# Kernel tuning notes

Measured on AMD Instinct MI355X. Metric: run time of the kernel, lower is better.

Reference implementation:

```python
import jax, jax.numpy as jnp
import numpy as np

ROUNDS = 64   # sequential hash rounds
HIDDEN = 256  # state width (bits) and square matrix size
B = 65536     # batch of independent inputs being hashed in parallel


def setup_inputs() -> dict:
    key = jax.random.key(0)
    k1, k2, k3 = jax.random.split(key, 3)
    # state bits in {0,1}, shape [B, HIDDEN]
    state = jax.random.randint(k1, (B, HIDDEN), 0, 2).astype(jnp.float32)
    # ternary matrices in {-1,0,1} (bytes % 3 - 1 in the original), [ROUNDS, HIDDEN, HIDDEN]
    matrices = (jax.random.randint(k2, (ROUNDS, HIDDEN, HIDDEN), 0, 3) - 1).astype(jnp.float32)
    # per-round noise bits in {0,1}, [ROUNDS, HIDDEN]
    noise = jax.random.randint(k3, (ROUNDS, HIDDEN), 0, 2).astype(jnp.float32)
    return {"state": state, "matrices": matrices, "noise": noise}


def reference(state, matrices, noise):
    # Each round: state = floor(state @ W_r^T + noise_r) mod 2
    def step(s, wn):
        W, n = wn  # W: [HIDDEN, HIDDEN], n: [HIDDEN]
        s = jnp.remainder(jnp.floor(jnp.matmul(s, W.T) + n), 2.0)
        return s, None

    out, _ = jax.lax.scan(step, state, (matrices, noise))
    return out  # [B, HIDDEN] final bit state
```

## Files before the change

kernel.cpp:

```cpp
#include <hip/hip_runtime.h>
#include <stdint.h>

#define ROUNDS 64
#define HIDDEN 256
#define BATCH  65536
#define NSUP   16

typedef int   v4i  __attribute__((ext_vector_type(4)));
typedef int   v8i  __attribute__((ext_vector_type(8)));
typedef float v16f __attribute__((ext_vector_type(16)));
typedef unsigned long long u64;


#define WB_OFF   0u
#define NB_OFF   524288u
#define WPK_OFF  526336u
#define NF_OFF   1050624u

__host__ __device__ constexpr int rho(int n) {
  return 4 * (n >> 4) + (n & 3) + 8 * ((n >> 2) & 3);
}

__host__ __device__ constexpr float bias_q(int q) {
  return (q == 0) ? 6291456.0f
       : (q == 1) ? 393216.0f
       : (q == 2) ? 24576.0f
                  : 1536.0f;
}

__global__ __launch_bounds__(256) void bitpack(const float* __restrict__ mat,
                                               const float* __restrict__ noi,
                                               u64* __restrict__ wb,
                                               u64* __restrict__ nb) {
  unsigned blk = blockIdx.x;
  if (blk >= 16384u) {
    unsigned tg = (blk - 16384u) * 256u + threadIdx.x;
    u64 m = __ballot(noi[tg] != 0.f);
    if ((threadIdx.x & 63u) == 0u) nb[tg >> 6] = m;
    return;
  }
  unsigned tg = blk * 256u + threadIdx.x;
  u64 m = __ballot(mat[tg] != 0.f);
  if ((threadIdx.x & 63u) == 0u) wb[tg >> 6] = m;
}

__device__ __forceinline__ void fold_stream(u64 (&A)[256][5],
                                            u64 (&tbl)[64][16][5],
                                            u64 (&avec)[4],
                                            const u64* __restrict__ inM,
                                            const u64* __restrict__ inV,
                                            int base, int count,
                                            int tid, int w, int i) {
  A[i][w] = inM[(size_t)base * 1024 + i * 4 + w];
  if (tid < 4) avec[tid] = inV[base * 4 + tid];
  u64 brP[4];
  u64 bwP;
  {
    const u64* Bm = inM + (size_t)(base + 1) * 1024;
#pragma unroll
    for (int q = 0; q < 4; ++q) brP[q] = Bm[i * 4 + q];
    bwP = (tid < 256) ? inV[(size_t)(base + 1) * 4 + (i >> 6)] : 0ull;
  }
  __syncthreads();

  for (int j = 1; j < count; ++j) {
    const u64 br0 = brP[0], br1 = brP[1], br2 = brP[2], br3 = brP[3];
    const u64 bwc = bwP;
    if (j + 1 < count) {
      const u64* Bm = inM + (size_t)(base + j + 1) * 1024;
#pragma unroll
      for (int q = 0; q < 4; ++q) brP[q] = Bm[i * 4 + q];
      bwP = (tid < 256) ? inV[(size_t)(base + j + 1) * 4 + (i >> 6)] : 0ull;
    }
    u64 av0 = avec[0], av1 = avec[1], av2 = avec[2], av3 = avec[3];

    {
      const int c = tid >> 4, m = tid & 15;
      u64 t0 = 0, t1 = 0, t2 = 0, t3 = 0;
#pragma unroll
      for (int jj = 0; jj < 4; ++jj)
        if (m & (1 << jj)) {
          t0 ^= A[4 * c + jj][0]; t1 ^= A[4 * c + jj][1];
          t2 ^= A[4 * c + jj][2]; t3 ^= A[4 * c + jj][3];
        }
      tbl[c][m][0] = t0; tbl[c][m][1] = t1; tbl[c][m][2] = t2; tbl[c][m][3] = t3;
    }
    __syncthreads();

    const u64 brr[4] = {br0, br1, br2, br3};
    u64 a0 = 0, a1 = 0, a2 = 0, a3 = 0;
#pragma unroll
    for (int c = 0; c < 64; c += 4) {
      unsigned n0 = (unsigned)(brr[(c + 0) >> 4] >> (((c + 0) & 15) * 4)) & 15u;
      unsigned n1 = (unsigned)(brr[(c + 1) >> 4] >> (((c + 1) & 15) * 4)) & 15u;
      unsigned n2 = (unsigned)(brr[(c + 2) >> 4] >> (((c + 2) & 15) * 4)) & 15u;
      unsigned n3 = (unsigned)(brr[(c + 3) >> 4] >> (((c + 3) & 15) * 4)) & 15u;
      a0 ^= tbl[c + 0][n0][w];
      a1 ^= tbl[c + 1][n1][w];
      a2 ^= tbl[c + 2][n2][w];
      a3 ^= tbl[c + 3][n3][w];
    }
    u64 acc = (a0 ^ a1) ^ (a2 ^ a3);

    u64 mask = 0;
    if (tid < 256) {
      int p = __popcll(br0 & av0) + __popcll(br1 & av1) +
              __popcll(br2 & av2) + __popcll(br3 & av3);
      int bit = ((int)((bwc >> (i & 63)) & 1ull)) ^ (p & 1);
      mask = __ballot(bit);
    }
    __syncthreads();
    A[i][w] = acc;
    if (tid < 256 && (i & 63) == 0) avec[i >> 6] = mask;
    __syncthreads();
  }
}

__global__ __launch_bounds__(1024) void fold16(const u64* __restrict__ wb,
                                               const u64* __restrict__ nb,
                                               uint32_t* __restrict__ wpk,
                                               float* __restrict__ nf) {
  __shared__ u64 A[256][5];
  __shared__ u64 tbl[64][16][5];
  __shared__ u64 avec[4];
  const int tid = threadIdx.x;
  const int g = blockIdx.x;

  fold_stream(A, tbl, avec, wb, nb, 4 * g, 4, tid, tid >> 8, tid & 255);

#pragma unroll
  for (int it = 0; it < 2; ++it) {
    unsigned tg = (unsigned)it * 1024u + tid;
    unsigned kwin = tg & 7u, row = tg >> 3;
    uint32_t wd[4] = {0, 0, 0, 0};
#pragma unroll
    for (int n = 0; n < 32; ++n) {
      int k = (int)kwin * 32 + rho(n);
      uint32_t bit = (uint32_t)((A[row][k >> 6] >> (k & 63)) & 1ull);
      wd[n >> 3] |= (bit * 2u) << ((n & 7) * 4);
    }
    unsigned mt = row >> 5, lhh = kwin & 1u, ks = kwin >> 1;
    unsigned lane = lhh * 32u + (row & 31u);
    *(uint4*)(wpk + ((((unsigned)g * 32u + mt * 4u + ks) * 64u + lane) << 2)) =
        make_uint4(wd[0], wd[1], wd[2], wd[3]);
  }
  if (tid < 256) {
    unsigned j = tid & 15u, lhh = (tid >> 4) & 1u, mt = (unsigned)tid >> 5;
    unsigned row = mt * 32u + (j & 3u) + 8u * (j >> 2) + 4u * lhh;
    nf[(unsigned)g * 256u + tid] = (float)((avec[row >> 6] >> (row & 63u)) & 1ull);
  }
}

__global__ __launch_bounds__(512, 4) void hash16(const uint32_t* __restrict__ wpk,
                                                 const float* __restrict__ nf,
                                                 const float* __restrict__ sta,
                                                 float* __restrict__ out) {
  __shared__ uint8_t T[2][8][128][16];
  const int t = threadIdx.x;
  const int wv = __builtin_amdgcn_readfirstlane(t >> 6);
  const int lane = t & 63;
  const int l31 = lane & 31;
  const int lh = lane >> 5;
  const int el0 = blockIdx.x * 128;

#pragma unroll
  for (int i = 0; i < 16; ++i) {
    unsigned flat = (unsigned)i * 512u + t;
    unsigned el = flat >> 6, k4 = flat & 63u;
    float4 f = ((const float4*)(sta + (size_t)el0 * 256))[flat];
    uint32_t v = ((f.x != 0.f) ? 0x2u : 0u) | ((f.y != 0.f) ? 0x20u : 0u) |
                 ((f.z != 0.f) ? 0x200u : 0u) | ((f.w != 0.f) ? 0x2000u : 0u);
    unsigned KB = k4 >> 3, k4c = k4 & 7u;
    unsigned byteoff = (k4c & 1u) * 8u + 2u * (k4c >> 1);
    *(uint16_t*)&T[0][KB][el][byteoff] = (uint16_t)v;
  }
  __syncthreads();

  v4i ap[4];
  {
    const uint32_t* wb = wpk + ((wv * 4) << 8);
#pragma unroll
    for (int ks = 0; ks < 4; ++ks) ap[ks] = *(const v4i*)(wb + ks * 256 + lane * 4);
  }
  v16f NZ = *(const v16f*)(nf + (wv * 2 + lh) * 16);

  for (int r = 0; r < NSUP; ++r) {
    const int rb = r & 1, nx = rb ^ 1;
    v16f acc[4];
    __builtin_amdgcn_s_setprio(1);
#pragma unroll
    for (int ks = 0; ks < 4; ++ks) {
      v8i A8 = __builtin_shufflevector(ap[ks], ap[ks], 0, 1, 2, 3, -1, -1, -1, -1);
      const int kb = 2 * ks + lh;
#pragma unroll
      for (int tn = 0; tn < 4; ++tn) {
        v4i b4 = *(const v4i*)&T[rb][kb][tn * 32 + l31][0];
        v8i B8 = __builtin_shufflevector(b4, b4, 0, 1, 2, 3, -1, -1, -1, -1);
        acc[tn] = __builtin_amdgcn_mfma_scale_f32_32x32x64_f8f6f4(
            A8, B8, (ks == 0) ? NZ : acc[tn], 4, 4, 0, 127, 0, 127);
      }
    }
    __builtin_amdgcn_s_setprio(0);

    {
      const int rn = (r + 1) & (NSUP - 1);
      const uint32_t* wb = wpk + (((rn * 8 + wv) * 4) << 8);
#pragma unroll
      for (int ks = 0; ks < 4; ++ks) ap[ks] = *(const v4i*)(wb + ks * 256 + lane * 4);
      NZ = *(const v16f*)(nf + ((rn * 8 + wv) * 2 + lh) * 16);
    }

#pragma unroll
    for (int tn = 0; tn < 4; ++tn) {
#define PB(j)                                                          \
  (__builtin_bit_cast(uint32_t, acc[tn][j] + bias_q((j) & 3)) &        \
   (2u << (4 * ((j) & 3))))
      uint32_t u0 = PB(0) | PB(1) | PB(2) | PB(3);
      uint32_t u1 = PB(4) | PB(5) | PB(6) | PB(7);
      uint32_t u2 = PB(8) | PB(9) | PB(10) | PB(11);
      uint32_t u3 = PB(12) | PB(13) | PB(14) | PB(15);
#undef PB
      *(uint2*)&T[nx][wv][tn * 32 + l31][lh * 8] =
          make_uint2(u0 | (u1 << 16), u2 | (u3 << 16));
    }

    __syncthreads();
  }

#pragma unroll
  for (int i = 0; i < 16; ++i) {
    unsigned flat = (unsigned)i * 512u + t;
    unsigned el = flat >> 6, k4 = flat & 63u;
    unsigned KB = k4 >> 3, k4c = k4 & 7u;
    unsigned byteoff = (k4c & 1u) * 8u + 2u * (k4c >> 1);
    uint32_t v = *(const uint16_t*)&T[0][KB][el][byteoff];
    float4 o = make_float4((float)((v >> 1) & 1u), (float)((v >> 5) & 1u),
                           (float)((v >> 9) & 1u), (float)((v >> 13) & 1u));
    ((float4*)(out + (size_t)el0 * 256))[flat] = o;
  }
}

extern "C" void kernel_launch(void* const* d_in, const int* in_sizes, int n_in,
                              void* d_out, int out_size, void* d_ws, size_t ws_size,
                              hipStream_t stream) {
  const float* sta = (const float*)d_in[0];
  const float* mat = (const float*)d_in[1];
  const float* noi = (const float*)d_in[2];
  uint8_t* wsb = (uint8_t*)d_ws;

  u64* Wb       = (u64*)(wsb + WB_OFF);
  u64* nb       = (u64*)(wsb + NB_OFF);
  uint32_t* wpk = (uint32_t*)(wsb + WPK_OFF);
  float* nf     = (float*)(wsb + NF_OFF);

  bitpack<<<16448, 256, 0, stream>>>(mat, noi, Wb, nb);
  fold16<<<16, 1024, 0, stream>>>(Wb, nb, wpk, nf);
  hash16<<<512, 512, 0, stream>>>(wpk, nf, sta, (float*)d_out);
}
```

Baseline: 207.2 us.

## Fuse matrix/noise bit-packing into the fold kernel and drop the intermediate buffer

Removes the separate bitpack kernel and has each of the 16 fold blocks ballot-pack its own four rounds of float matrices and noise directly into shared memory. This saves a kernel launch and the global write and read of the packed bit matrices. The fold loop now reads the next operand from shared memory instead of prefetching it from global memory. The trade-off is that the 16 MB float matrix read now runs on only 16 workgroups, where before it was spread across the whole GPU, so it may be bandwidth-limited per CU.

New measurement: 273.7 us. +32.1%, slower.

```diff
diff --git a/kernel.cpp b/kernel.cpp
--- a/kernel.cpp
+++ b/kernel.cpp
@@ -12,10 +12,8 @@
 typedef unsigned long long u64;
 
 
-#define WB_OFF   0u
-#define NB_OFF   524288u
-#define WPK_OFF  526336u
-#define NF_OFF   1050624u
+#define WPK_OFF  0u
+#define NF_OFF   524288u
 
 __host__ __device__ constexpr int rho(int n) {
   return 4 * (n >> 4) + (n & 3) + 8 * ((n >> 2) & 3);
@@ -28,51 +26,43 @@
                   : 1536.0f;
 }
 
-__global__ __launch_bounds__(256) void bitpack(const float* __restrict__ mat,
-                                               const float* __restrict__ noi,
-                                               u64* __restrict__ wb,
-                                               u64* __restrict__ nb) {
-  unsigned blk = blockIdx.x;
-  if (blk >= 16384u) {
-    unsigned tg = (blk - 16384u) * 256u + threadIdx.x;
-    u64 m = __ballot(noi[tg] != 0.f);
-    if ((threadIdx.x & 63u) == 0u) nb[tg >> 6] = m;
-    return;
-  }
-  unsigned tg = blk * 256u + threadIdx.x;
-  u64 m = __ballot(mat[tg] != 0.f);
-  if ((threadIdx.x & 63u) == 0u) wb[tg >> 6] = m;
-}
-
-__device__ __forceinline__ void fold_stream(u64 (&A)[256][5],
-                                            u64 (&tbl)[64][16][5],
-                                            u64 (&avec)[4],
-                                            const u64* __restrict__ inM,
-                                            const u64* __restrict__ inV,
-                                            int base, int count,
-                                            int tid, int w, int i) {
-  A[i][w] = inM[(size_t)base * 1024 + i * 4 + w];
-  if (tid < 4) avec[tid] = inV[base * 4 + tid];
-  u64 brP[4];
-  u64 bwP;
+__global__ __launch_bounds__(1024) void foldpack16(const float* __restrict__ mat,
+                                                   const float* __restrict__ noi,
+                                                   uint32_t* __restrict__ wpk,
+                                                   float* __restrict__ nf) {
+  __shared__ u64 WB[4][256][5];
+  __shared__ u64 NBv[4][4];
+  __shared__ u64 A[256][5];
+  __shared__ u64 tbl[64][16][5];
+  __shared__ u64 avec[4];
+  const int tid = threadIdx.x;
+  const int g = blockIdx.x;
+  const int w = tid >> 8;
+  const int i = tid & 255;
+
   {
-    const u64* Bm = inM + (size_t)(base + 1) * 1024;
-#pragma unroll
-    for (int q = 0; q < 4; ++q) brP[q] = Bm[i * 4 + q];
-    bwP = (tid < 256) ? inV[(size_t)(base + 1) * 4 + (i >> 6)] : 0ull;
+    const float* src = mat + (size_t)g * 262144;
+#pragma unroll 8
+    for (int it = 0; it < 256; ++it) {
+      unsigned e = (unsigned)it * 1024u + (unsigned)tid;
+      u64 m = __ballot(src[e] != 0.f);
+      if ((tid & 63) == 0) WB[e >> 16][(e >> 8) & 255][(e >> 6) & 3] = m;
+    }
+    u64 m = __ballot(noi[(size_t)g * 1024 + tid] != 0.f);
+    if ((tid & 63) == 0) NBv[tid >> 8][(tid >> 6) & 3] = m;
   }
   __syncthreads();
 
-  for (int j = 1; j < count; ++j) {
-    const u64 br0 = brP[0], br1 = brP[1], br2 = brP[2], br3 = brP[3];
-    const u64 bwc = bwP;
-    if (j + 1 < count) {
-      const u64* Bm = inM + (size_t)(base + j + 1) * 1024;
-#pragma unroll
-      for (int q = 0; q < 4; ++q) brP[q] = Bm[i * 4 + q];
-      bwP = (tid < 256) ? inV[(size_t)(base + j + 1) * 4 + (i >> 6)] : 0ull;
-    }
-    u64 av0 = avec[0], av1 = avec[1], av2 = avec[2], av3 = avec[3];
+  A[i][w] = WB[0][i][w];
+  if (tid < 4) avec[tid] = NBv[0][tid];
+  __syncthreads();
+
+#pragma unroll
+  for (int j = 1; j < 4; ++j) {
+    const u64 br0 = WB[j][i][0], br1 = WB[j][i][1],
+              br2 = WB[j][i][2], br3 = WB[j][i][3];
+    const u64 bwc = NBv[j][i >> 6];
+    const u64 av0 = avec[0], av1 = avec[1], av2 = avec[2], av3 = avec[3];
 
     {
       const int c = tid >> 4, m = tid & 15;
@@ -100,7 +90,7 @@
       a2 ^= tbl[c + 2][n2][w];
       a3 ^= tbl[c + 3][n3][w];
     }
-    u64 acc = (a0 ^ a1) ^ (a2 ^ a3);
+    const u64 acc = (a0 ^ a1) ^ (a2 ^ a3);
 
     u64 mask = 0;
     if (tid < 256) {
@@ -114,19 +104,6 @@
     if (tid < 256 && (i & 63) == 0) avec[i >> 6] = mask;
     __syncthreads();
   }
-}
-
-__global__ __launch_bounds__(1024) void fold16(const u64* __restrict__ wb,
-                                               const u64* __restrict__ nb,
-                                               uint32_t* __restrict__ wpk,
-                                               float* __restrict__ nf) {
-  __shared__ u64 A[256][5];
-  __shared__ u64 tbl[64][16][5];
-  __shared__ u64 avec[4];
-  const int tid = threadIdx.x;
-  const int g = blockIdx.x;
-
-  fold_stream(A, tbl, avec, wb, nb, 4 * g, 4, tid, tid >> 8, tid & 255);
 
 #pragma unroll
   for (int it = 0; it < 2; ++it) {
@@ -248,12 +225,9 @@
   const float* noi = (const float*)d_in[2];
   uint8_t* wsb = (uint8_t*)d_ws;
 
-  u64* Wb       = (u64*)(wsb + WB_OFF);
-  u64* nb       = (u64*)(wsb + NB_OFF);
   uint32_t* wpk = (uint32_t*)(wsb + WPK_OFF);
   float* nf     = (float*)(wsb + NF_OFF);
 
-  bitpack<<<16448, 256, 0, stream>>>(mat, noi, Wb, nb);
-  fold16<<<16, 1024, 0, stream>>>(Wb, nb, wpk, nf);
+  foldpack16<<<16, 1024, 0, stream>>>(mat, noi, wpk, nf);
   hash16<<<512, 512, 0, stream>>>(wpk, nf, sta, (float*)d_out);
 }
```

## Fold eight rounds per affine map and prepack state bits in bitpack kernel

Applied to the files above, without the earlier changes.

Each folded affine map now composes 8 rounds instead of 4, so the hash kernel runs 8 super-rounds of MFMA work instead of 16 and the fold kernel runs 8 blocks each folding 8 rounds. The state bit extraction moves into the bitpack launch, producing packed 32-bit words that the hash kernel spreads into its LDS layout with bit tricks instead of reading the float state itself. The trade-offs are a longer serial fold chain per block, an extra packed buffer in the workspace, and extra blocks in bitpack.

New measurement: 229.6 us. 1.11x slower.

```diff
diff --git a/kernel.cpp b/kernel.cpp
--- a/kernel.cpp
+++ b/kernel.cpp
@@ -4,7 +4,7 @@
 #define ROUNDS 64
 #define HIDDEN 256
 #define BATCH  65536
-#define NSUP   16
+#define NSUP   8
 
 typedef int   v4i  __attribute__((ext_vector_type(4)));
 typedef int   v8i  __attribute__((ext_vector_type(8)));
@@ -12,10 +12,11 @@
 typedef unsigned long long u64;
 
 
-#define WB_OFF   0u
-#define NB_OFF   524288u
-#define WPK_OFF  526336u
-#define NF_OFF   1050624u
+#define SPK_OFF  0u
+#define WB_OFF   2097152u
+#define NB_OFF   2621440u
+#define WPK_OFF  2623488u
+#define NF_OFF   2885632u
 
 __host__ __device__ constexpr int rho(int n) {
   return 4 * (n >> 4) + (n & 3) + 8 * ((n >> 2) & 3);
@@ -28,20 +29,49 @@
                   : 1536.0f;
 }
 
+__device__ __forceinline__ u64 spread16(uint32_t p) {
+  u64 t = p;
+  t = (t | (t << 24)) & 0x000000FF000000FFull;
+  t = (t | (t << 12)) & 0x000F000F000F000Full;
+  t = (t | (t << 6))  & 0x0303030303030303ull;
+  t = (t | (t << 3))  & 0x1111111111111111ull;
+  return t << 1;
+}
+
 __global__ __launch_bounds__(256) void bitpack(const float* __restrict__ mat,
                                                const float* __restrict__ noi,
+                                               const float* __restrict__ sta,
                                                u64* __restrict__ wb,
-                                               u64* __restrict__ nb) {
+                                               u64* __restrict__ nb,
+                                               uint32_t* __restrict__ spk) {
   unsigned blk = blockIdx.x;
-  if (blk >= 16384u) {
+  if (blk < 16384u) {
+    unsigned tg = blk * 256u + threadIdx.x;
+    u64 m = __ballot(mat[tg] != 0.f);
+    if ((threadIdx.x & 63u) == 0u) wb[tg >> 6] = m;
+    return;
+  }
+  if (blk < 16448u) {
     unsigned tg = (blk - 16384u) * 256u + threadIdx.x;
     u64 m = __ballot(noi[tg] != 0.f);
     if ((threadIdx.x & 63u) == 0u) nb[tg >> 6] = m;
     return;
   }
-  unsigned tg = blk * 256u + threadIdx.x;
-  u64 m = __ballot(mat[tg] != 0.f);
-  if ((threadIdx.x & 63u) == 0u) wb[tg >> 6] = m;
+  unsigned tg = (blk - 16448u) * 256u + threadIdx.x;
+  unsigned el = tg >> 3, KB = tg & 7u;
+  const float4* s4 = (const float4*)(sta + (size_t)el * 256 + KB * 32);
+  float4 f[8];
+#pragma unroll
+  for (int q = 0; q < 8; ++q) f[q] = s4[q];
+  uint32_t bits = 0;
+#pragma unroll
+  for (int q = 0; q < 8; ++q) {
+    bits |= (f[q].x != 0.f ? 1u : 0u) << (4 * q + 0);
+    bits |= (f[q].y != 0.f ? 1u : 0u) << (4 * q + 1);
+    bits |= (f[q].z != 0.f ? 1u : 0u) << (4 * q + 2);
+    bits |= (f[q].w != 0.f ? 1u : 0u) << (4 * q + 3);
+  }
+  spk[(el >> 7) * 1024u + KB * 128u + (el & 127u)] = bits;
 }
 
 __device__ __forceinline__ void fold_stream(u64 (&A)[256][5],
@@ -116,17 +146,17 @@
   }
 }
 
-__global__ __launch_bounds__(1024) void fold16(const u64* __restrict__ wb,
-                                               const u64* __restrict__ nb,
-                                               uint32_t* __restrict__ wpk,
-                                               float* __restrict__ nf) {
+__global__ __launch_bounds__(1024) void fold8(const u64* __restrict__ wb,
+                                              const u64* __restrict__ nb,
+                                              uint32_t* __restrict__ wpk,
+                                              float* __restrict__ nf) {
   __shared__ u64 A[256][5];
   __shared__ u64 tbl[64][16][5];
   __shared__ u64 avec[4];
   const int tid = threadIdx.x;
   const int g = blockIdx.x;
 
-  fold_stream(A, tbl, avec, wb, nb, 4 * g, 4, tid, tid >> 8, tid & 255);
+  fold_stream(A, tbl, avec, wb, nb, 8 * g, 8, tid, tid >> 8, tid & 255);
 
 #pragma unroll
   for (int it = 0; it < 2; ++it) {
@@ -151,10 +181,10 @@
   }
 }
 
-__global__ __launch_bounds__(512, 4) void hash16(const uint32_t* __restrict__ wpk,
-                                                 const float* __restrict__ nf,
-                                                 const float* __restrict__ sta,
-                                                 float* __restrict__ out) {
+__global__ __launch_bounds__(512, 4) void hash8(const uint32_t* __restrict__ wpk,
+                                                const float* __restrict__ nf,
+                                                const uint32_t* __restrict__ spk,
+                                                float* __restrict__ out) {
   __shared__ uint8_t T[2][8][128][16];
   const int t = threadIdx.x;
   const int wv = __builtin_amdgcn_readfirstlane(t >> 6);
@@ -163,16 +193,22 @@
   const int lh = lane >> 5;
   const int el0 = blockIdx.x * 128;
 
-#pragma unroll
-  for (int i = 0; i < 16; ++i) {
-    unsigned flat = (unsigned)i * 512u + t;
-    unsigned el = flat >> 6, k4 = flat & 63u;
-    float4 f = ((const float4*)(sta + (size_t)el0 * 256))[flat];
-    uint32_t v = ((f.x != 0.f) ? 0x2u : 0u) | ((f.y != 0.f) ? 0x20u : 0u) |
-                 ((f.z != 0.f) ? 0x200u : 0u) | ((f.w != 0.f) ? 0x2000u : 0u);
-    unsigned KB = k4 >> 3, k4c = k4 & 7u;
-    unsigned byteoff = (k4c & 1u) * 8u + 2u * (k4c >> 1);
-    *(uint16_t*)&T[0][KB][el][byteoff] = (uint16_t)v;
+  {
+    const uint32_t* sb = spk + (unsigned)blockIdx.x * 1024u;
+#pragma unroll
+    for (int it = 0; it < 2; ++it) {
+      unsigned idx = (unsigned)it * 512u + t;
+      uint32_t bits = sb[idx];
+      unsigned KB = idx >> 7, el = idx & 127u;
+      uint32_t pl = bits & 0x0F0F0F0Fu;
+      pl = (pl | (pl >> 4)) & 0x00FF00FFu; pl = (pl | (pl >> 8)) & 0xFFFFu;
+      uint32_t ph = (bits >> 4) & 0x0F0F0F0Fu;
+      ph = (ph | (ph >> 4)) & 0x00FF00FFu; ph = (ph | (ph >> 8)) & 0xFFFFu;
+      u64 lo = spread16(pl), hi = spread16(ph);
+      *(uint4*)&T[0][KB][el][0] =
+          make_uint4((uint32_t)lo, (uint32_t)(lo >> 32),
+                     (uint32_t)hi, (uint32_t)(hi >> 32));
+    }
   }
   __syncthreads();
 
@@ -248,12 +284,13 @@
   const float* noi = (const float*)d_in[2];
   uint8_t* wsb = (uint8_t*)d_ws;
 
+  uint32_t* spk = (uint32_t*)(wsb + SPK_OFF);
   u64* Wb       = (u64*)(wsb + WB_OFF);
   u64* nb       = (u64*)(wsb + NB_OFF);
   uint32_t* wpk = (uint32_t*)(wsb + WPK_OFF);
   float* nf     = (float*)(wsb + NF_OFF);
 
-  bitpack<<<16448, 256, 0, stream>>>(mat, noi, Wb, nb);
-  fold16<<<16, 1024, 0, stream>>>(Wb, nb, wpk, nf);
-  hash16<<<512, 512, 0, stream>>>(wpk, nf, sta, (float*)d_out);
-}
+  bitpack<<<18496, 256, 0, stream>>>(mat, noi, sta, Wb, nb, spk);
+  fold8<<<8, 1024, 0, stream>>>(Wb, nb, wpk, nf);
+  hash8<<<512, 512, 0, stream>>>(wpk, nf, spk, (float*)d_out);
+}
```
